# Kernel optimization log

Measured on AMD Instinct MI355X. Metric: run time of the kernel, lower is better.

The kernel has to match this reference:

```python
import jax, jax.numpy as jnp
import numpy as np

B, S, D, H, NH, E, K = 16, 512, 768, 3072, 12, 7, 2
DPH = D // NH  # 64
EPS = 1e-12


def setup_inputs() -> dict:
    key = jax.random.key(0)
    ks = jax.random.split(key, 12)
    p = lambda k, shape: (0.02 * jax.random.normal(k, shape, dtype=jnp.float32))
    return {
        "hidden_states": jax.random.normal(ks[0], (B, S, D), dtype=jnp.float32),
        "attention_mask": jnp.ones((B, S), dtype=jnp.int32),
        "ln1_g": jnp.ones((D,), jnp.float32), "ln1_b": jnp.zeros((D,), jnp.float32),
        "wq": p(ks[1], (D, D)), "bq": jnp.zeros((D,), jnp.float32),
        "wk": p(ks[2], (D, D)), "bk": jnp.zeros((D,), jnp.float32),
        "wv": p(ks[3], (D, D)), "bv": jnp.zeros((D,), jnp.float32),
        "wo": p(ks[4], (D, D)), "bo": jnp.zeros((D,), jnp.float32),
        "gate_w": p(ks[5], (D, E)), "gate_b": jnp.zeros((E,), jnp.float32),
        "w1": p(ks[6], (E, D, H)), "b1": jnp.zeros((E, H), jnp.float32),
        "w2": p(ks[7], (E, H, D)), "b2": jnp.zeros((E, D), jnp.float32),
        "ln2_g": jnp.ones((D,), jnp.float32), "ln2_b": jnp.zeros((D,), jnp.float32),
    }


def layer_norm(x, g, b):
    m = jnp.mean(x, axis=-1, keepdims=True)
    v = jnp.mean(jnp.square(x - m), axis=-1, keepdims=True)
    return g * (x - m) * jax.lax.rsqrt(v + EPS) + b


def reference(hidden_states, attention_mask, ln1_g, ln1_b, wq, bq, wk, bk, wv, bv,
              wo, bo, gate_w, gate_b, w1, b1, w2, b2, ln2_g, ln2_b):
    b, s, d = hidden_states.shape
    x = layer_norm(hidden_states, ln1_g, ln1_b)

    # DistilBERT MultiHeadSelfAttention (dropout = identity in eval)
    q = (x @ wq + bq).reshape(b, s, NH, DPH) / jnp.sqrt(jnp.float32(DPH))
    k = (x @ wk + bk).reshape(b, s, NH, DPH)
    v = (x @ wv + bv).reshape(b, s, NH, DPH)
    scores = jnp.einsum("bqhd,bkhd->bhqk", q, k)  # [B,NH,S,S]
    neg = jnp.finfo(scores.dtype).min
    scores = jnp.where(attention_mask[:, None, None, :] != 0, scores, neg)
    probs = jax.nn.softmax(scores, axis=-1)
    ctx = jnp.einsum("bhqk,bkhd->bqhd", probs, v).reshape(b, s, d)
    attn = ctx @ wo + bo
    attn = attn + hidden_states  # residual (attention_dropout = identity)

    x2 = layer_norm(attn, ln2_g, ln2_b)

    # MoE FFN: top-k sparse gating over E experts, dense compute of all experts
    gate_logits = x2 @ gate_w + gate_b  # [B,S,E]
    _, topk_idx = jax.lax.top_k(gate_logits, K)
    keep = jnp.sum(jax.nn.one_hot(topk_idx, E, dtype=gate_logits.dtype), axis=-2)  # [B,S,E]
    masked = jnp.where(keep > 0, gate_logits, jnp.finfo(gate_logits.dtype).min)
    gate_weights = jax.nn.softmax(masked, axis=-1)  # zeros outside top-k

    mid = jax.nn.gelu(jnp.einsum("bsd,edh->bseh", x2, w1) + b1, approximate=False)
    expert_out = jnp.einsum("bseh,ehd->bsed", mid, w2) + b2  # [B,S,E,D]
    ffn = jnp.einsum("bsed,bse->bsd", expert_out, gate_weights)

    out = ffn + attn  # output_dropout = identity
    return out, gate_weights
```

## Files before the change

### kernel.cpp

```cpp
#include <hip/hip_runtime.h>
#include <hip/hip_bf16.h>
#include <math.h>

#define TB 16
#define TS 512
#define TD 768
#define TH 3072
#define TNH 12
#define TE 7
#define TT (TB*TS)

typedef __bf16 bf16x8_t __attribute__((ext_vector_type(8)));
typedef __bf16 bf16x4_t __attribute__((ext_vector_type(4)));
typedef float f32x4_t __attribute__((ext_vector_type(4)));

#define NEGINF (-__builtin_huge_valf())

#define O_APL   0ULL
#define O_VT0   0ULL
#define O_VT1   12582912ULL
#define O_CTXH  37748736ULL
#define O_CTXM  50331648ULL
#define O_QKH   62914560ULL
#define O_QKM   88080384ULL
#define O_VCOL  113246208ULL
#define O_BT    138412032ULL
#define O_META  149028864ULL
#define O_MIDG  150077440ULL
#define O_X2    62914560ULL
#define O_XG    75497472ULL
#define O_W1T   0ULL
#define O_W2T   33030144ULL
#define M_CNT   0
#define M_FILL  64
#define M_NRB   192
#define M_RB2E  256
#define M_TOKE  1024
#define M_TOKW  66560
#define M_RGW   201216
#define M_TSLOT 270336

#define NRB_MAX 135
#define ROWCAP  17280

__device__ __forceinline__ void async16(const void* g, void* l) {
  __builtin_amdgcn_global_load_lds(
      (const __attribute__((address_space(1))) void*)g,
      (__attribute__((address_space(3))) void*)l, 16, 0, 0);
}

__device__ __forceinline__ void split2(float x, __bf16& h, __bf16& m) {
  h = (__bf16)x;
  m = (__bf16)(x - (float)h);
}

__device__ __forceinline__ float block_sum256(float v, float* red4) {
  #pragma unroll
  for (int o = 32; o > 0; o >>= 1) v += __shfl_down(v, o, 64);
  int lane = threadIdx.x & 63, wv = threadIdx.x >> 6;
  if (lane == 0) red4[wv] = v;
  __syncthreads();
  float r = red4[0] + red4[1] + red4[2] + red4[3];
  __syncthreads();
  return r;
}

__global__ void init_meta_k(int* cnt) {
  if (threadIdx.x < TE) cnt[threadIdx.x] = 0;
}

__global__ __launch_bounds__(256) void ln1_split_k(const float* __restrict__ in,
                                                   const float* __restrict__ g,
                                                   const float* __restrict__ bb,
                                                   __bf16* __restrict__ P) {
  __shared__ float red4[4];
  const size_t SA = (size_t)TT * TD;
  int row = blockIdx.x, tid = threadIdx.x;
  const float* x = in + (size_t)row * TD;
  float v0 = x[tid], v1 = x[tid + 256], v2 = x[tid + 512];
  float sum = block_sum256(v0 + v1 + v2, red4);
  float mean = sum * (1.0f / 768.0f);
  float d0 = v0 - mean, d1 = v1 - mean, d2 = v2 - mean;
  float var = block_sum256(d0*d0 + d1*d1 + d2*d2, red4) * (1.0f / 768.0f);
  float rs = rsqrtf(var + 1e-12f);
  float xn[3] = { g[tid]       * (d0 * rs) + bb[tid],
                  g[tid + 256] * (d1 * rs) + bb[tid + 256],
                  g[tid + 512] * (d2 * rs) + bb[tid + 512] };
  #pragma unroll
  for (int i = 0; i < 3; ++i) {
    __bf16 h, m; split2(xn[i], h, m);
    size_t o = (size_t)row * TD + tid + 256 * i;
    P[o] = h; P[SA + o] = m;
  }
}

__global__ void tpose_split2_k(const float* __restrict__ W0, const float* __restrict__ W1,
                               const float* __restrict__ W2,
                               __bf16* __restrict__ BT, size_t SB, int roffmul) {
  __shared__ float tile[32][33];
  const float* W = (blockIdx.z == 0) ? W0 : (blockIdx.z == 1) ? W1 : W2;
  int roff = roffmul * (int)blockIdx.z * TD;
  int c0 = blockIdx.x * 32, r0 = blockIdx.y * 32;
  int tx = threadIdx.x, ty = threadIdx.y;
  #pragma unroll
  for (int i = 0; i < 32; i += 8)
    tile[ty + i][tx] = W[(size_t)(r0 + ty + i) * TD + c0 + tx];
  __syncthreads();
  #pragma unroll
  for (int i = 0; i < 32; i += 8) {
    float x = tile[tx][ty + i];
    __bf16 h, m; split2(x, h, m);
    size_t o = (size_t)(roff + c0 + ty + i) * TD + r0 + tx;
    BT[o] = h; BT[SB + o] = m;
  }
}

template<int EPI>
__global__ __launch_bounds__(256) void gemm_split4_k(
    const __bf16* __restrict__ A0, const __bf16* __restrict__ A1,
    const __bf16* __restrict__ Bpl, size_t SB,
    const float* __restrict__ bi0, const float* __restrict__ bi1, const float* __restrict__ bi2,
    const float* __restrict__ resid, float* __restrict__ C,
    __bf16* __restrict__ qh_out, __bf16* __restrict__ qm_out, float* __restrict__ vout)
{
  __shared__ __align__(16) __bf16 As[2][4096];
  __shared__ __align__(16) __bf16 Bs[2][4096];
  const __bf16* Ap[2] = {A0, A1};
  int n0 = blockIdx.x * 128, m0 = blockIdx.y * 128;
  int tid = threadIdx.x;
  int wave = tid >> 6, lane = tid & 63;
  int wr = wave >> 1, wc = wave & 1;
  int lm = lane & 15, q = lane >> 4;
  int qs = (q ^ ((lm >> 1) & 3)) * 8;
  f32x4_t acc[4][4];
  #pragma unroll
  for (int i = 0; i < 4; ++i)
    #pragma unroll
    for (int j = 0; j < 4; ++j) { f32x4_t z = {0.f,0.f,0.f,0.f}; acc[i][j] = z; }
  for (int k0 = 0; k0 < TD; k0 += 32) {
    #pragma unroll
    for (int it = 0; it < 2; ++it) {
      int f = it * 256 + tid; int r = f >> 2;
      int c8 = ((f & 3) ^ ((f >> 3) & 3)) * 8;
      #pragma unroll
      for (int p = 0; p < 2; ++p) {
        async16(Ap[p] + (size_t)(m0 + r) * TD + k0 + c8, &As[p][f * 8]);
        async16(Bpl + p * SB + (size_t)(n0 + r) * TD + k0 + c8, &Bs[p][f * 8]);
      }
    }
    __syncthreads();
    bf16x8_t af[2][4];
    #pragma unroll
    for (int pa = 0; pa < 2; ++pa)
      #pragma unroll
      for (int i = 0; i < 4; ++i)
        af[pa][i] = *(const bf16x8_t*)(&As[pa][(wr*64 + i*16 + lm) * 32 + qs]);
    #pragma unroll
    for (int pb = 0; pb < 2; ++pb) {
      bf16x8_t bfr[4];
      #pragma unroll
      for (int j = 0; j < 4; ++j)
        bfr[j] = *(const bf16x8_t*)(&Bs[pb][(wc*64 + j*16 + lm) * 32 + qs]);
      #pragma unroll
      for (int pa = 0; pa < 2; ++pa)
        #pragma unroll
        for (int i = 0; i < 4; ++i)
          #pragma unroll
          for (int j = 0; j < 4; ++j)
            acc[i][j] = __builtin_amdgcn_mfma_f32_16x16x32_bf16(af[pa][i], bfr[j], acc[i][j], 0, 0, 0);
    }
    __syncthreads();
  }
  #pragma unroll
  for (int i = 0; i < 4; ++i) {
    #pragma unroll
    for (int j = 0; j < 4; ++j) {
      #pragma unroll
      for (int r = 0; r < 4; ++r) {
        int row = m0 + wr*64 + i*16 + q*4 + r;
        int col = n0 + wc*64 + j*16 + lm;
        float v = acc[i][j][r];
        if (EPI == 0) {
          float bias = (col < 768) ? bi0[col] : (col < 1536) ? bi1[col - 768] : bi2[col - 1536];
          v += bias;
          if (col < 768) v *= 0.125f;
          if (col < 1536) {
            __bf16 hh = (__bf16)v; float r1 = v - (float)hh;
            qh_out[(size_t)row * 1536 + col] = hh;
            qm_out[(size_t)row * 1536 + col] = (__bf16)r1;
          } else {
            vout[(size_t)row * TD + (col - 1536)] = v;
          }
        } else {
          v += bi0[col] + resid[(size_t)row * TD + col];
          C[(size_t)row * TD + col] = v;
        }
      }
    }
  }
}

__global__ void vT_split2_k(const float* __restrict__ vcol,
                            __bf16* __restrict__ v0, __bf16* __restrict__ v1) {
  __shared__ float tile[32][33];
  int s0 = blockIdx.x * 32, d0 = blockIdx.y * 32, bh = blockIdx.z;
  int b = bh / 12, h = bh - b * 12;
  int tx = threadIdx.x, ty = threadIdx.y;
  #pragma unroll
  for (int i = 0; i < 32; i += 8)
    tile[ty + i][tx] = vcol[(size_t)(b * TS + s0 + ty + i) * TD + h * 64 + d0 + tx];
  __syncthreads();
  #pragma unroll
  for (int i = 0; i < 32; i += 8) {
    float x = tile[tx][ty + i];
    __bf16 hh, mm; split2(x, hh, mm);
    size_t o = (size_t)(bh * 64 + d0 + ty + i) * TS + s0 + tx;
    v0[o] = hh; v1[o] = mm;
  }
}

#define AST 72
__global__ __launch_bounds__(256) void attn_mfma_k(
    const __bf16* __restrict__ qkh, const __bf16* __restrict__ qkm,
    const __bf16* __restrict__ vT0, const __bf16* __restrict__ vT1,
    const int* __restrict__ mask,
    __bf16* __restrict__ ch, __bf16* __restrict__ cm)
{
  __shared__ __align__(16) __bf16 KS[2][64 * AST];
  __shared__ __align__(16) __bf16 VS[2][64 * AST];
  __shared__ __align__(16) __bf16 PS[2][64 * AST];
  __shared__ float maskadd[512];
  int qt = blockIdx.x, h = blockIdx.y, b = blockIdx.z;
  int tid = threadIdx.x, w = tid >> 6, lane = tid & 63;
  int lm = lane & 15, quad = lane >> 4;
  int t0 = b * TS, t0q = t0 + qt * 64, bh = b * TNH + h;
  for (int i = tid; i < 512; i += 256)
    maskadd[i] = (mask[t0 + i] != 0) ? 0.0f : -1e30f;
  #pragma unroll
  for (int it = 0; it < 2; ++it) {
    int f = it * 256 + tid, r = f >> 3, c8 = (f & 7) * 8;
    *(uint4*)&PS[0][r * AST + c8] = *(const uint4*)(qkh + (size_t)(t0q + r) * 1536 + h * 64 + c8);
    *(uint4*)&PS[1][r * AST + c8] = *(const uint4*)(qkm + (size_t)(t0q + r) * 1536 + h * 64 + c8);
  }
  __syncthreads();
  bf16x8_t qf[2][2];
  #pragma unroll
  for (int p = 0; p < 2; ++p)
    #pragma unroll
    for (int ks = 0; ks < 2; ++ks)
      qf[p][ks] = *(const bf16x8_t*)&PS[p][(w * 16 + lm) * AST + ks * 32 + quad * 8];
  __syncthreads();
  f32x4_t Oacc[4];
  #pragma unroll
  for (int j = 0; j < 4; ++j) { f32x4_t z = {0.f,0.f,0.f,0.f}; Oacc[j] = z; }
  float mst[4], lst[4];
  #pragma unroll
  for (int r = 0; r < 4; ++r) { mst[r] = -3.0e38f; lst[r] = 0.0f; }

  for (int kc = 0; kc < 8; ++kc) {
    #pragma unroll
    for (int it = 0; it < 2; ++it) {
      int f = it * 256 + tid, r = f >> 3, c8 = (f & 7) * 8;
      size_t ksrc = (size_t)(t0 + kc * 64 + r) * 1536 + 768 + h * 64 + c8;
      *(uint4*)&KS[0][r * AST + c8] = *(const uint4*)(qkh + ksrc);
      *(uint4*)&KS[1][r * AST + c8] = *(const uint4*)(qkm + ksrc);
      size_t vsrc = (size_t)(bh * 64 + r) * TS + kc * 64 + c8;
      *(uint4*)&VS[0][r * AST + c8] = *(const uint4*)(vT0 + vsrc);
      *(uint4*)&VS[1][r * AST + c8] = *(const uint4*)(vT1 + vsrc);
    }
    __syncthreads();
    f32x4_t sacc[4];
    #pragma unroll
    for (int j = 0; j < 4; ++j) { f32x4_t z = {0.f,0.f,0.f,0.f}; sacc[j] = z; }
    #pragma unroll
    for (int ks = 0; ks < 2; ++ks) {
      bf16x8_t kh_[4], km_[4];
      #pragma unroll
      for (int jn = 0; jn < 4; ++jn) {
        kh_[jn] = *(const bf16x8_t*)&KS[0][(jn*16 + lm) * AST + ks*32 + quad*8];
        km_[jn] = *(const bf16x8_t*)&KS[1][(jn*16 + lm) * AST + ks*32 + quad*8];
      }
      #pragma unroll
      for (int jn = 0; jn < 4; ++jn)
        sacc[jn] = __builtin_amdgcn_mfma_f32_16x16x32_bf16(qf[0][ks], kh_[jn], sacc[jn], 0,0,0);
      #pragma unroll
      for (int jn = 0; jn < 4; ++jn)
        sacc[jn] = __builtin_amdgcn_mfma_f32_16x16x32_bf16(qf[0][ks], km_[jn], sacc[jn], 0,0,0);
      #pragma unroll
      for (int jn = 0; jn < 4; ++jn)
        sacc[jn] = __builtin_amdgcn_mfma_f32_16x16x32_bf16(qf[1][ks], kh_[jn], sacc[jn], 0,0,0);
    }
    float s[4][4];
    #pragma unroll
    for (int jn = 0; jn < 4; ++jn)
      #pragma unroll
      for (int r = 0; r < 4; ++r)
        s[jn][r] = sacc[jn][r] + maskadd[kc*64 + jn*16 + lm];
    float alpha[4];
    #pragma unroll
    for (int r = 0; r < 4; ++r) {
      float rmax = fmaxf(fmaxf(s[0][r], s[1][r]), fmaxf(s[2][r], s[3][r]));
      #pragma unroll
      for (int mk = 1; mk < 16; mk <<= 1)
        rmax = fmaxf(rmax, __shfl_xor(rmax, mk, 64));
      float mnew = fmaxf(mst[r], rmax);
      alpha[r] = expf(mst[r] - mnew);
      mst[r] = mnew;
      float psum = 0.0f;
      #pragma unroll
      for (int jn = 0; jn < 4; ++jn) {
        float p = expf(s[jn][r] - mnew);
        s[jn][r] = p;
        psum += p;
      }
      #pragma unroll
      for (int mk = 1; mk < 16; mk <<= 1)
        psum += __shfl_xor(psum, mk, 64);
      lst[r] = lst[r] * alpha[r] + psum;
    }
    #pragma unroll
    for (int jn = 0; jn < 4; ++jn)
      #pragma unroll
      for (int r = 0; r < 4; ++r)
        Oacc[jn][r] *= alpha[r];
    #pragma unroll
    for (int jn = 0; jn < 4; ++jn)
      #pragma unroll
      for (int r = 0; r < 4; ++r) {
        __bf16 ph, pm; split2(s[jn][r], ph, pm);
        int pa = (w*16 + quad*4 + r) * AST + jn*16 + lm;
        PS[0][pa] = ph; PS[1][pa] = pm;
      }
    __syncthreads();
    #pragma unroll
    for (int ks = 0; ks < 2; ++ks) {
      bf16x8_t af[2];
      #pragma unroll
      for (int p = 0; p < 2; ++p)
        af[p] = *(const bf16x8_t*)&PS[p][(w*16 + lm) * AST + ks*32 + quad*8];
      bf16x8_t vf[2][4];
      #pragma unroll
      for (int p = 0; p < 2; ++p)
        #pragma unroll
        for (int jn = 0; jn < 4; ++jn)
          vf[p][jn] = *(const bf16x8_t*)&VS[p][(jn*16 + lm) * AST + ks*32 + quad*8];
      #pragma unroll
      for (int jn = 0; jn < 4; ++jn) {
        Oacc[jn] = __builtin_amdgcn_mfma_f32_16x16x32_bf16(af[0], vf[0][jn], Oacc[jn], 0,0,0);
        Oacc[jn] = __builtin_amdgcn_mfma_f32_16x16x32_bf16(af[0], vf[1][jn], Oacc[jn], 0,0,0);
        Oacc[jn] = __builtin_amdgcn_mfma_f32_16x16x32_bf16(af[1], vf[0][jn], Oacc[jn], 0,0,0);
        Oacc[jn] = __builtin_amdgcn_mfma_f32_16x16x32_bf16(af[1], vf[1][jn], Oacc[jn], 0,0,0);
      }
    }
    __syncthreads();
  }
  float linv[4];
  #pragma unroll
  for (int r = 0; r < 4; ++r) linv[r] = 1.0f / lst[r];
  #pragma unroll
  for (int jn = 0; jn < 4; ++jn)
    #pragma unroll
    for (int r = 0; r < 4; ++r) {
      float o = Oacc[jn][r] * linv[r];
      __bf16 hh, mm; split2(o, hh, mm);
      size_t oo = (size_t)(t0q + w*16 + quad*4 + r) * TD + h*64 + jn*16 + lm;
      ch[oo] = hh; cm[oo] = mm;
    }
}

__global__ __launch_bounds__(256) void ln2_gate_k(const float* __restrict__ attn,
                                                  const float* __restrict__ g,
                                                  const float* __restrict__ bb,
                                                  const float* __restrict__ gw,
                                                  const float* __restrict__ gb,
                                                  __bf16* __restrict__ x2,
                                                  float* __restrict__ gates,
                                                  int* __restrict__ tok_e,
                                                  float* __restrict__ tok_w) {
  __shared__ float red4[4];
  __shared__ float redc[4][7];
  int row = blockIdx.x, tid = threadIdx.x;
  const float* x = attn + (size_t)row * TD;
  float v0 = x[tid], v1 = x[tid + 256], v2 = x[tid + 512];
  float sum = block_sum256(v0 + v1 + v2, red4);
  float mean = sum * (1.0f / 768.0f);
  float d0 = v0 - mean, d1 = v1 - mean, d2 = v2 - mean;
  float var = block_sum256(d0*d0 + d1*d1 + d2*d2, red4) * (1.0f / 768.0f);
  float rs = rsqrtf(var + 1e-12f);
  float xn0 = g[tid]       * (d0 * rs) + bb[tid];
  float xn1 = g[tid + 256] * (d1 * rs) + bb[tid + 256];
  float xn2 = g[tid + 512] * (d2 * rs) + bb[tid + 512];
  __bf16* xo = x2 + (size_t)row * TD;
  xo[tid] = (__bf16)xn0; xo[tid + 256] = (__bf16)xn1; xo[tid + 512] = (__bf16)xn2;
  float p[7];
  const float* w0 = gw + (size_t)tid * 7;
  const float* w1p = gw + (size_t)(tid + 256) * 7;
  const float* w2p = gw + (size_t)(tid + 512) * 7;
  #pragma unroll
  for (int e = 0; e < 7; ++e) p[e] = xn0 * w0[e] + xn1 * w1p[e] + xn2 * w2p[e];
  #pragma unroll
  for (int e = 0; e < 7; ++e)
    #pragma unroll
    for (int o = 32; o > 0; o >>= 1) p[e] += __shfl_down(p[e], o, 64);
  int lane = tid & 63, wv = tid >> 6;
  if (lane == 0) {
    #pragma unroll
    for (int e = 0; e < 7; ++e) redc[wv][e] = p[e];
  }
  __syncthreads();
  if (tid == 0) {
    float l[7];
    #pragma unroll
    for (int e = 0; e < 7; ++e)
      l[e] = redc[0][e] + redc[1][e] + redc[2][e] + redc[3][e] + gb[e];
    int i1 = 0;
    for (int e = 1; e < 7; ++e) if (l[e] > l[i1]) i1 = e;
    int i2 = -1;
    for (int e = 0; e < 7; ++e) if (e != i1 && (i2 < 0 || l[e] > l[i2])) i2 = e;
    float m = l[i1];
    float e1 = expf(l[i1] - m), e2 = expf(l[i2] - m);
    float inv = 1.0f / (e1 + e2);
    float g1 = e1 * inv, g2 = e2 * inv;
    float* go = gates + (size_t)row * 7;
    #pragma unroll
    for (int e = 0; e < 7; ++e) go[e] = 0.0f;
    go[i1] = g1; go[i2] = g2;
    tok_e[row * 2] = i1; tok_e[row * 2 + 1] = i2;
    tok_w[row * 2] = g1; tok_w[row * 2 + 1] = g2;
  }
}

__global__ __launch_bounds__(256) void hist_k(const int* __restrict__ tok_e,
                                              int* __restrict__ cnt) {
  __shared__ int hloc[TE];
  int i = blockIdx.x * 256 + threadIdx.x;
  int e = tok_e[i];
  if (threadIdx.x < TE) hloc[threadIdx.x] = 0;
  __syncthreads();
  #pragma unroll
  for (int ee = 0; ee < TE; ++ee) {
    unsigned long long m = __ballot(e == ee);
    if ((threadIdx.x & 63) == 0 && m) atomicAdd(&hloc[ee], (int)__popcll(m));
  }
  __syncthreads();
  if (threadIdx.x < TE) atomicAdd(&cnt[threadIdx.x], hloc[threadIdx.x]);
}

__global__ void prefix_k(const int* __restrict__ cnt, int* __restrict__ fill,
                         int* __restrict__ nrb_p, int* __restrict__ rb2e) {
  __shared__ int start[TE + 1];
  if (threadIdx.x == 0) {
    int acc = 0;
    for (int e = 0; e < TE; ++e) {
      start[e] = acc;
      int nb = (cnt[e] + 127) >> 7;
      fill[e] = acc * 128;
      acc += nb;
    }
    start[TE] = acc;
    nrb_p[0] = acc;
  }
  __syncthreads();
  for (int b = threadIdx.x; b < start[TE]; b += blockDim.x) {
    int e = 0;
    while (start[e + 1] <= b) ++e;
    rb2e[b] = e;
  }
}

__global__ __launch_bounds__(256) void slot_assign_k(const int* __restrict__ tok_e,
                                                     const float* __restrict__ tok_w,
                                                     int* __restrict__ fill,
                                                     int* __restrict__ tok_slot,
                                                     float* __restrict__ row_gw) {
  __shared__ int wcnt[4][TE];
  __shared__ int wbase[4][TE];
  int i = blockIdx.x * 256 + threadIdx.x;
  int e = tok_e[i];
  int lane = threadIdx.x & 63, wv = threadIdx.x >> 6;
  unsigned long long lt = (1ULL << lane) - 1ULL;
  int myrank = 0;
  #pragma unroll
  for (int ee = 0; ee < TE; ++ee) {
    unsigned long long m = __ballot(e == ee);
    if (e == ee) myrank = (int)__popcll(m & lt);
    if (lane == 0) wcnt[wv][ee] = (int)__popcll(m);
  }
  __syncthreads();
  if (threadIdx.x < TE) {
    int ee = threadIdx.x;
    int c0 = wcnt[0][ee], c1 = wcnt[1][ee], c2 = wcnt[2][ee], c3 = wcnt[3][ee];
    int base = atomicAdd(&fill[ee], c0 + c1 + c2 + c3);
    wbase[0][ee] = base;
    wbase[1][ee] = base + c0;
    wbase[2][ee] = base + c0 + c1;
    wbase[3][ee] = base + c0 + c1 + c2;
  }
  __syncthreads();
  int slot = wbase[wv][e] + myrank;
  tok_slot[i] = slot;
  row_gw[slot] = tok_w[i];
}

__global__ __launch_bounds__(192) void copy_xg_k(const __bf16* __restrict__ x2,
                                                 const int* __restrict__ tok_slot,
                                                 __bf16* __restrict__ xg) {
  int t = blockIdx.x, tid = threadIdx.x;
  int j = tid / 96, c = tid - j * 96;
  int s = tok_slot[t * 2 + j];
  *(uint4*)(xg + (size_t)s * TD + c * 8) =
      *(const uint4*)(x2 + (size_t)t * TD + c * 8);
}

__global__ void transpose_cast_k(const float* __restrict__ in, __bf16* __restrict__ out,
                                 int R, int C) {
  __shared__ float tile[32][33];
  size_t zoff = (size_t)blockIdx.z * R * C;
  const float* ip = in + zoff;
  __bf16* op = out + zoff;
  int c0 = blockIdx.x * 32, r0 = blockIdx.y * 32;
  int tx = threadIdx.x, ty = threadIdx.y;
  #pragma unroll
  for (int i = 0; i < 32; i += 8)
    tile[ty + i][tx] = ip[(size_t)(r0 + ty + i) * C + c0 + tx];
  __syncthreads();
  #pragma unroll
  for (int i = 0; i < 32; i += 8)
    op[(size_t)(c0 + ty + i) * R + r0 + tx] = (__bf16)tile[tx][ty + i];
}

__global__ __launch_bounds__(256) void gemm1_k(
    const __bf16* __restrict__ xg, const __bf16* __restrict__ w1T,
    const float* __restrict__ b1, const int* __restrict__ rb2e,
    const int* __restrict__ nrb_p, int cb, __bf16* __restrict__ midg)
{
  int rb = cb + blockIdx.y;
  if (rb >= nrb_p[0]) return;
  int e = rb2e[rb];
  __shared__ __align__(16) __bf16 As[2][4096];
  __shared__ __align__(16) __bf16 Bs[2][4096];
  const __bf16* A = xg + (size_t)rb * 128 * TD;
  const __bf16* BT = w1T + (size_t)e * TH * TD;
  const float* be = b1 + (size_t)e * TH;
  int n0 = blockIdx.x * 128;
  int tid = threadIdx.x;
  int wave = tid >> 6, lane = tid & 63;
  int wr = wave >> 1, wc = wave & 1;
  int lm = lane & 15, q = lane >> 4;
  int qs = (q ^ ((lm >> 1) & 3)) * 8;
  f32x4_t acc[4][4];
  #pragma unroll
  for (int i = 0; i < 4; ++i)
    #pragma unroll
    for (int j = 0; j < 4; ++j) { f32x4_t z = {0.f,0.f,0.f,0.f}; acc[i][j] = z; }

  int r_ = tid >> 2;
  int c8_ = ((tid & 3) ^ ((tid >> 3) & 3)) * 8;
  int r2_ = (256 + tid) >> 2;
  int c82_ = (((256 + tid) & 3) ^ (((256 + tid) >> 3) & 3)) * 8;

  #define G1_STAGE(buf, k0) do { \
    async16(A + (size_t)r_ * TD + (k0) + c8_, &As[buf][tid * 8]); \
    async16(BT + (size_t)(n0 + r_) * TD + (k0) + c8_, &Bs[buf][tid * 8]); \
    async16(A + (size_t)r2_ * TD + (k0) + c82_, &As[buf][(256 + tid) * 8]); \
    async16(BT + (size_t)(n0 + r2_) * TD + (k0) + c82_, &Bs[buf][(256 + tid) * 8]); \
  } while (0)

  const int NT = TD / 32;
  G1_STAGE(0, 0);
  __syncthreads();
  int cur = 0;
  for (int t = 0; t < NT; ++t) {
    if (t + 1 < NT) G1_STAGE(cur ^ 1, (t + 1) * 32);
    bf16x8_t af[4], bfr[4];
    #pragma unroll
    for (int i = 0; i < 4; ++i) af[i]  = *(const bf16x8_t*)(&As[cur][(wr*64 + i*16 + lm)*32 + qs]);
    #pragma unroll
    for (int j = 0; j < 4; ++j) bfr[j] = *(const bf16x8_t*)(&Bs[cur][(wc*64 + j*16 + lm)*32 + qs]);
    #pragma unroll
    for (int i = 0; i < 4; ++i)
      #pragma unroll
      for (int j = 0; j < 4; ++j)
        acc[i][j] = __builtin_amdgcn_mfma_f32_16x16x32_bf16(af[i], bfr[j], acc[i][j], 0, 0, 0);
    __syncthreads();
    cur ^= 1;
  }
  #undef G1_STAGE

  #pragma unroll
  for (int i = 0; i < 4; ++i) {
    #pragma unroll
    for (int j = 0; j < 4; ++j) {
      #pragma unroll
      for (int r = 0; r < 4; ++r) {
        int row = wr*64 + i*16 + q*4 + r;
        int col = n0 + wc*64 + j*16 + lm;
        float v = acc[i][j][r] + be[col];
        v = 0.5f * v * (1.0f + erff(v * 0.70710678118654752f));
        midg[(size_t)(blockIdx.y * 128 + row) * TH + col] = (__bf16)v;
      }
    }
  }
}

__global__ __launch_bounds__(256) void gemm2_k(
    const __bf16* __restrict__ midg, const __bf16* __restrict__ w2T,
    const float* __restrict__ b2, const int* __restrict__ rb2e,
    const int* __restrict__ nrb_p, const float* __restrict__ row_gw,
    int cb, __bf16* __restrict__ part)
{
  int rb = cb + blockIdx.y;
  if (rb >= nrb_p[0]) return;
  int e = rb2e[rb];
  __shared__ __align__(16) __bf16 As[2][4096];
  __shared__ __align__(16) __bf16 Bs[2][4096];
  const __bf16* A = midg + (size_t)blockIdx.y * 128 * TH;
  const __bf16* BT = w2T + (size_t)e * TD * TH;
  const float* be = b2 + (size_t)e * TD;
  int n0 = blockIdx.x * 128;
  int tid = threadIdx.x;
  int wave = tid >> 6, lane = tid & 63;
  int wr = wave >> 1, wc = wave & 1;
  int lm = lane & 15, q = lane >> 4;
  int qs = (q ^ ((lm >> 1) & 3)) * 8;
  f32x4_t acc[4][4];
  #pragma unroll
  for (int i = 0; i < 4; ++i)
    #pragma unroll
    for (int j = 0; j < 4; ++j) { f32x4_t z = {0.f,0.f,0.f,0.f}; acc[i][j] = z; }

  int r_ = tid >> 2;
  int c8_ = ((tid & 3) ^ ((tid >> 3) & 3)) * 8;
  int r2_ = (256 + tid) >> 2;
  int c82_ = (((256 + tid) & 3) ^ (((256 + tid) >> 3) & 3)) * 8;

  #define G2_STAGE(buf, k0) do { \
    async16(A + (size_t)r_ * TH + (k0) + c8_, &As[buf][tid * 8]); \
    async16(BT + (size_t)(n0 + r_) * TH + (k0) + c8_, &Bs[buf][tid * 8]); \
    async16(A + (size_t)r2_ * TH + (k0) + c82_, &As[buf][(256 + tid) * 8]); \
    async16(BT + (size_t)(n0 + r2_) * TH + (k0) + c82_, &Bs[buf][(256 + tid) * 8]); \
  } while (0)

  const int NT = TH / 32;
  G2_STAGE(0, 0);
  __syncthreads();
  int cur = 0;
  for (int t = 0; t < NT; ++t) {
    if (t + 1 < NT) G2_STAGE(cur ^ 1, (t + 1) * 32);
    bf16x8_t af[4], bfr[4];
    #pragma unroll
    for (int i = 0; i < 4; ++i) af[i]  = *(const bf16x8_t*)(&As[cur][(wr*64 + i*16 + lm)*32 + qs]);
    #pragma unroll
    for (int j = 0; j < 4; ++j) bfr[j] = *(const bf16x8_t*)(&Bs[cur][(wc*64 + j*16 + lm)*32 + qs]);
    #pragma unroll
    for (int i = 0; i < 4; ++i)
      #pragma unroll
      for (int j = 0; j < 4; ++j)
        acc[i][j] = __builtin_amdgcn_mfma_f32_16x16x32_bf16(af[i], bfr[j], acc[i][j], 0, 0, 0);
    __syncthreads();
    cur ^= 1;
  }
  #undef G2_STAGE

  #pragma unroll
  for (int i = 0; i < 4; ++i) {
    #pragma unroll
    for (int r = 0; r < 4; ++r) {
      int row = wr*64 + i*16 + q*4 + r;
      int grow = rb * 128 + row;
      float gwt = row_gw[grow];
      #pragma unroll
      for (int j = 0; j < 4; ++j) {
        int col = n0 + wc*64 + j*16 + lm;
        part[(size_t)grow * TD + col] = (__bf16)(gwt * (acc[i][j][r] + be[col]));
      }
    }
  }
}

__global__ __launch_bounds__(192) void gather_k(const __bf16* __restrict__ part,
                                                const int* __restrict__ tok_slot,
                                                float* __restrict__ outp) {
  int t = blockIdx.x, tid = threadIdx.x;
  int s0 = tok_slot[t * 2], s1 = tok_slot[t * 2 + 1];
  int c = tid * 4;
  float4 o = *(float4*)(outp + (size_t)t * TD + c);
  bf16x4_t p0 = *(const bf16x4_t*)(part + (size_t)s0 * TD + c);
  bf16x4_t p1 = *(const bf16x4_t*)(part + (size_t)s1 * TD + c);
  o.x += (float)p0[0] + (float)p1[0];
  o.y += (float)p0[1] + (float)p1[1];
  o.z += (float)p0[2] + (float)p1[2];
  o.w += (float)p0[3] + (float)p1[3];
  *(float4*)(outp + (size_t)t * TD + c) = o;
}

extern "C" void kernel_launch(void* const* d_in, const int* in_sizes, int n_in,
                              void* d_out, int out_size, void* d_ws, size_t ws_size,
                              hipStream_t stream) {
  (void)in_sizes; (void)n_in; (void)out_size;
  const float* hidden = (const float*)d_in[0];
  const int*   mask   = (const int*)d_in[1];
  const float* ln1_g  = (const float*)d_in[2];
  const float* ln1_b  = (const float*)d_in[3];
  const float* wq = (const float*)d_in[4];  const float* bq = (const float*)d_in[5];
  const float* wk = (const float*)d_in[6];  const float* bk = (const float*)d_in[7];
  const float* wv = (const float*)d_in[8];  const float* bv = (const float*)d_in[9];
  const float* wo = (const float*)d_in[10]; const float* bo = (const float*)d_in[11];
  const float* gate_w = (const float*)d_in[12];
  const float* gate_b = (const float*)d_in[13];
  const float* w1 = (const float*)d_in[14];
  const float* b1 = (const float*)d_in[15];
  const float* w2 = (const float*)d_in[16];
  const float* b2 = (const float*)d_in[17];
  const float* ln2_g = (const float*)d_in[18];
  const float* ln2_b = (const float*)d_in[19];

  float* outp  = (float*)d_out;
  float* gates = (float*)d_out + (size_t)TT * TD;

  char* ws = (char*)d_ws;
  __bf16* Apl  = (__bf16*)(ws + O_APL);
  __bf16* vT0p = (__bf16*)(ws + O_VT0);
  __bf16* vT1p = (__bf16*)(ws + O_VT1);
  __bf16* ctxh = (__bf16*)(ws + O_CTXH);
  __bf16* ctxm = (__bf16*)(ws + O_CTXM);
  __bf16* qkh  = (__bf16*)(ws + O_QKH);
  __bf16* qkm  = (__bf16*)(ws + O_QKM);
  float*  vcol = (float*)(ws + O_VCOL);
  __bf16* BTp  = (__bf16*)(ws + O_BT);
  __bf16* x2   = (__bf16*)(ws + O_X2);
  __bf16* xg   = (__bf16*)(ws + O_XG);
  __bf16* w1T  = (__bf16*)(ws + O_W1T);
  __bf16* w2T  = (__bf16*)(ws + O_W2T);
  char*   meta = ws + O_META;
  int*   cnt      = (int*)(meta + M_CNT);
  int*   fill     = (int*)(meta + M_FILL);
  int*   nrb_p    = (int*)(meta + M_NRB);
  int*   rb2e     = (int*)(meta + M_RB2E);
  int*   tok_e    = (int*)(meta + M_TOKE);
  float* tok_w    = (float*)(meta + M_TOKW);
  float* row_gw   = (float*)(meta + M_RGW);
  int*   tok_slot = (int*)(meta + M_TSLOT);
  __bf16* midg = (__bf16*)(ws + O_MIDG);

  long long midcap = (long long)ws_size - (long long)O_MIDG;
  int crb = (int)(midcap / (128LL * TH * 2));
  if (crb < 1) crb = 1;
  if (crb > NRB_MAX) crb = NRB_MAX;

  const size_t SA = (size_t)TT * TD;

  init_meta_k<<<1, 64, 0, stream>>>(cnt);
  ln1_split_k<<<TT, 256, 0, stream>>>(hidden, ln1_g, ln1_b, Apl);
  tpose_split2_k<<<dim3(24, 24, 3), dim3(32, 8), 0, stream>>>(
      wq, wk, wv, BTp, (size_t)2304 * TD, 1);
  gemm_split4_k<0><<<dim3(18, 64), 256, 0, stream>>>(
      Apl, Apl + SA, BTp, (size_t)2304 * TD,
      bq, bk, bv, nullptr, nullptr, qkh, qkm, vcol);
  vT_split2_k<<<dim3(16, 2, 192), dim3(32, 8), 0, stream>>>(vcol, vT0p, vT1p);
  attn_mfma_k<<<dim3(8, TNH, TB), 256, 0, stream>>>(
      qkh, qkm, vT0p, vT1p, mask, ctxh, ctxm);
  tpose_split2_k<<<dim3(24, 24, 1), dim3(32, 8), 0, stream>>>(
      wo, wo, wo, BTp, (size_t)TD * TD, 0);
  gemm_split4_k<1><<<dim3(6, 64), 256, 0, stream>>>(
      ctxh, ctxm, BTp, (size_t)TD * TD,
      bo, nullptr, nullptr, hidden, outp, nullptr, nullptr, nullptr);
  ln2_gate_k<<<TT, 256, 0, stream>>>(outp, ln2_g, ln2_b, gate_w, gate_b, x2, gates,
                                     tok_e, tok_w);
  hist_k<<<64, 256, 0, stream>>>(tok_e, cnt);
  prefix_k<<<1, 192, 0, stream>>>(cnt, fill, nrb_p, rb2e);
  slot_assign_k<<<64, 256, 0, stream>>>(tok_e, tok_w, fill, tok_slot, row_gw);
  copy_xg_k<<<TT, 192, 0, stream>>>(x2, tok_slot, xg);
  transpose_cast_k<<<dim3(TH / 32, TD / 32, TE), dim3(32, 8), 0, stream>>>(w1, w1T, TD, TH);
  transpose_cast_k<<<dim3(TD / 32, TH / 32, TE), dim3(32, 8), 0, stream>>>(w2, w2T, TH, TD);
  __bf16* part = xg;
  for (int cb = 0; cb < NRB_MAX; cb += crb) {
    int nb = NRB_MAX - cb; if (nb > crb) nb = crb;
    gemm1_k<<<dim3(TH / 128, nb), 256, 0, stream>>>(xg, w1T, b1, rb2e, nrb_p, cb, midg);
    gemm2_k<<<dim3(TD / 128, nb), 256, 0, stream>>>(midg, w2T, b2, rb2e, nrb_p,
                                                    row_gw, cb, part);
  }
  gather_k<<<TT, 192, 0, stream>>>(part, tok_slot, outp);
}
```

Before: 903.3 us.

## Triple-buffer FFN GEMM shared-memory pipeline with partial vmcnt waits

Both MoE FFN GEMM kernels move from a double-buffered LDS pipeline with a full __syncthreads per k-step to a three-stage ring buffer. Two tiles are kept in flight, each step waits only until the oldest tile has landed (vmcnt(4)), and there is a single barrier per step. Global pointers are bumped incrementally instead of recomputed. The goal is to hide global load latency behind MFMA work, at the cost of 50% more LDS per block, which may lower occupancy. The correctness of the ring depends on loop counts that divide evenly: 24 and 96 k-steps.

```diff
diff --git a/kernel.cpp b/kernel.cpp
--- a/kernel.cpp
+++ b/kernel.cpp
@@ -529,6 +529,30 @@
     op[(size_t)(c0 + ty + i) * R + r0 + tx] = (__bf16)tile[tx][ty + i];
 }
 
+
+#define FFN_STG(AS, BS, X) do { \
+    async16(pA1, &AS[X][tid * 8]);          async16(pB1, &BS[X][tid * 8]); \
+    async16(pA2, &AS[X][(256 + tid) * 8]);  async16(pB2, &BS[X][(256 + tid) * 8]); \
+    pA1 += 32; pB1 += 32; pA2 += 32; pB2 += 32; \
+  } while (0)
+
+#define FFN_COMP(AS, BS, X) do { \
+    bf16x8_t af[4], bfr[4]; \
+    _Pragma("unroll") \
+    for (int i = 0; i < 4; ++i) af[i]  = *(const bf16x8_t*)(&AS[X][(wr*64 + i*16 + lm)*32 + qs]); \
+    _Pragma("unroll") \
+    for (int j = 0; j < 4; ++j) bfr[j] = *(const bf16x8_t*)(&BS[X][(wc*64 + j*16 + lm)*32 + qs]); \
+    _Pragma("unroll") \
+    for (int i = 0; i < 4; ++i) \
+      _Pragma("unroll") \
+      for (int j = 0; j < 4; ++j) \
+        acc[i][j] = __builtin_amdgcn_mfma_f32_16x16x32_bf16(af[i], bfr[j], acc[i][j], 0, 0, 0); \
+  } while (0)
+
+#define WAITV4 asm volatile("s_waitcnt vmcnt(4)" ::: "memory")
+#define WAITV0 asm volatile("s_waitcnt vmcnt(0)" ::: "memory")
+#define BAR    __builtin_amdgcn_s_barrier()
+
 __global__ __launch_bounds__(256) void gemm1_k(
     const __bf16* __restrict__ xg, const __bf16* __restrict__ w1T,
     const float* __restrict__ b1, const int* __restrict__ rb2e,
@@ -537,8 +561,8 @@
   int rb = cb + blockIdx.y;
   if (rb >= nrb_p[0]) return;
   int e = rb2e[rb];
-  __shared__ __align__(16) __bf16 As[2][4096];
-  __shared__ __align__(16) __bf16 Bs[2][4096];
+  __shared__ __align__(16) __bf16 As[3][4096];
+  __shared__ __align__(16) __bf16 Bs[3][4096];
   const __bf16* A = xg + (size_t)rb * 128 * TD;
   const __bf16* BT = w1T + (size_t)e * TH * TD;
   const float* be = b1 + (size_t)e * TH;
@@ -558,34 +582,22 @@
   int c8_ = ((tid & 3) ^ ((tid >> 3) & 3)) * 8;
   int r2_ = (256 + tid) >> 2;
   int c82_ = (((256 + tid) & 3) ^ (((256 + tid) >> 3) & 3)) * 8;
-
-  #define G1_STAGE(buf, k0) do { \
-    async16(A + (size_t)r_ * TD + (k0) + c8_, &As[buf][tid * 8]); \
-    async16(BT + (size_t)(n0 + r_) * TD + (k0) + c8_, &Bs[buf][tid * 8]); \
-    async16(A + (size_t)r2_ * TD + (k0) + c82_, &As[buf][(256 + tid) * 8]); \
-    async16(BT + (size_t)(n0 + r2_) * TD + (k0) + c82_, &Bs[buf][(256 + tid) * 8]); \
-  } while (0)
+  const __bf16* pA1 = A + (size_t)r_ * TD + c8_;
+  const __bf16* pB1 = BT + (size_t)(n0 + r_) * TD + c8_;
+  const __bf16* pA2 = A + (size_t)r2_ * TD + c82_;
+  const __bf16* pB2 = BT + (size_t)(n0 + r2_) * TD + c82_;
 
   const int NT = TD / 32;
-  G1_STAGE(0, 0);
-  __syncthreads();
-  int cur = 0;
-  for (int t = 0; t < NT; ++t) {
-    if (t + 1 < NT) G1_STAGE(cur ^ 1, (t + 1) * 32);
-    bf16x8_t af[4], bfr[4];
-    #pragma unroll
-    for (int i = 0; i < 4; ++i) af[i]  = *(const bf16x8_t*)(&As[cur][(wr*64 + i*16 + lm)*32 + qs]);
-    #pragma unroll
-    for (int j = 0; j < 4; ++j) bfr[j] = *(const bf16x8_t*)(&Bs[cur][(wc*64 + j*16 + lm)*32 + qs]);
-    #pragma unroll
-    for (int i = 0; i < 4; ++i)
-      #pragma unroll
-      for (int j = 0; j < 4; ++j)
-        acc[i][j] = __builtin_amdgcn_mfma_f32_16x16x32_bf16(af[i], bfr[j], acc[i][j], 0, 0, 0);
-    __syncthreads();
-    cur ^= 1;
-  }
-  #undef G1_STAGE
+  FFN_STG(As, Bs, 0);
+  FFN_STG(As, Bs, 1);
+  for (int t = 0; t < NT - 3; t += 3) {
+    WAITV4; BAR; FFN_STG(As, Bs, 2); FFN_COMP(As, Bs, 0);
+    WAITV4; BAR; FFN_STG(As, Bs, 0); FFN_COMP(As, Bs, 1);
+    WAITV4; BAR; FFN_STG(As, Bs, 1); FFN_COMP(As, Bs, 2);
+  }
+  WAITV4; BAR; FFN_STG(As, Bs, 2); FFN_COMP(As, Bs, 0);
+  WAITV4; BAR; FFN_COMP(As, Bs, 1);
+  WAITV0; BAR; FFN_COMP(As, Bs, 2);
 
   #pragma unroll
   for (int i = 0; i < 4; ++i) {
@@ -612,8 +624,8 @@
   int rb = cb + blockIdx.y;
   if (rb >= nrb_p[0]) return;
   int e = rb2e[rb];
-  __shared__ __align__(16) __bf16 As[2][4096];
-  __shared__ __align__(16) __bf16 Bs[2][4096];
+  __shared__ __align__(16) __bf16 As[3][4096];
+  __shared__ __align__(16) __bf16 Bs[3][4096];
   const __bf16* A = midg + (size_t)blockIdx.y * 128 * TH;
   const __bf16* BT = w2T + (size_t)e * TD * TH;
   const float* be = b2 + (size_t)e * TD;
@@ -633,34 +645,22 @@
   int c8_ = ((tid & 3) ^ ((tid >> 3) & 3)) * 8;
   int r2_ = (256 + tid) >> 2;
   int c82_ = (((256 + tid) & 3) ^ (((256 + tid) >> 3) & 3)) * 8;
-
-  #define G2_STAGE(buf, k0) do { \
-    async16(A + (size_t)r_ * TH + (k0) + c8_, &As[buf][tid * 8]); \
-    async16(BT + (size_t)(n0 + r_) * TH + (k0) + c8_, &Bs[buf][tid * 8]); \
-    async16(A + (size_t)r2_ * TH + (k0) + c82_, &As[buf][(256 + tid) * 8]); \
-    async16(BT + (size_t)(n0 + r2_) * TH + (k0) + c82_, &Bs[buf][(256 + tid) * 8]); \
-  } while (0)
+  const __bf16* pA1 = A + (size_t)r_ * TH + c8_;
+  const __bf16* pB1 = BT + (size_t)(n0 + r_) * TH + c8_;
+  const __bf16* pA2 = A + (size_t)r2_ * TH + c82_;
+  const __bf16* pB2 = BT + (size_t)(n0 + r2_) * TH + c82_;
 
   const int NT = TH / 32;
-  G2_STAGE(0, 0);
-  __syncthreads();
-  int cur = 0;
-  for (int t = 0; t < NT; ++t) {
-    if (t + 1 < NT) G2_STAGE(cur ^ 1, (t + 1) * 32);
-    bf16x8_t af[4], bfr[4];
-    #pragma unroll
-    for (int i = 0; i < 4; ++i) af[i]  = *(const bf16x8_t*)(&As[cur][(wr*64 + i*16 + lm)*32 + qs]);
-    #pragma unroll
-    for (int j = 0; j < 4; ++j) bfr[j] = *(const bf16x8_t*)(&Bs[cur][(wc*64 + j*16 + lm)*32 + qs]);
-    #pragma unroll
-    for (int i = 0; i < 4; ++i)
-      #pragma unroll
-      for (int j = 0; j < 4; ++j)
-        acc[i][j] = __builtin_amdgcn_mfma_f32_16x16x32_bf16(af[i], bfr[j], acc[i][j], 0, 0, 0);
-    __syncthreads();
-    cur ^= 1;
-  }
-  #undef G2_STAGE
+  FFN_STG(As, Bs, 0);
+  FFN_STG(As, Bs, 1);
+  for (int t = 0; t < NT - 3; t += 3) {
+    WAITV4; BAR; FFN_STG(As, Bs, 2); FFN_COMP(As, Bs, 0);
+    WAITV4; BAR; FFN_STG(As, Bs, 0); FFN_COMP(As, Bs, 1);
+    WAITV4; BAR; FFN_STG(As, Bs, 1); FFN_COMP(As, Bs, 2);
+  }
+  WAITV4; BAR; FFN_STG(As, Bs, 2); FFN_COMP(As, Bs, 0);
+  WAITV4; BAR; FFN_COMP(As, Bs, 1);
+  WAITV0; BAR; FFN_COMP(As, Bs, 2);
 
   #pragma unroll
   for (int i = 0; i < 4; ++i) {
```

After: 886.7 us. Within noise of the previous version (-1.8%).
